# Optimization experiments

Measured on AMD Instinct MI355X. Metric: run time of the kernel, lower is better.

## Reference

```python
import jax, jax.numpy as jnp
import numpy as np

N = 1024
IN_CH = 128
EDGE_CH = 32
OUT_CH = 128


def setup_inputs() -> dict:
    key = jax.random.key(0)
    ks = jax.random.split(key, 8)
    return {
        "node_mat": jax.random.normal(ks[0], (N, IN_CH), dtype=jnp.float32),
        "adj": jax.random.uniform(ks[1], (N, N), dtype=jnp.float32),
        "edge_adj": jax.random.uniform(ks[2], (EDGE_CH, N, N), dtype=jnp.float32),
        "node_weight": jax.random.normal(ks[3], (IN_CH, OUT_CH), dtype=jnp.float32) * 0.05,
        "edge_lay_1": jax.random.normal(ks[4], (EDGE_CH, OUT_CH - 1), dtype=jnp.float32) * 0.05,
        "edge_lay_2": jax.random.normal(ks[5], (OUT_CH - 1, OUT_CH), dtype=jnp.float32) * 0.05,
        "root": jax.random.normal(ks[6], (IN_CH, OUT_CH), dtype=jnp.float32) * 0.05,
        "bias": jax.random.normal(ks[7], (OUT_CH,), dtype=jnp.float32) * 0.05,
    }


def reference(node_mat, adj, edge_adj, node_weight, edge_lay_1, edge_lay_2, root, bias):
    # node message passing: adj-weighted sum of transformed node features  [N, out]
    sum_filter_node_msgs = adj @ (node_mat @ node_weight)
    # edge MLP: 2-layer with ReLU, applied over the edge-channel axis
    # edge_adj: [E, N, N]; edge_lay_1: [E, out-1] -> h1: [out-1, N, N]
    h1 = jnp.maximum(jnp.einsum('enm,eb->bnm', edge_adj, edge_lay_1), 0.0)
    # h1: [out-1, N, N]; edge_lay_2: [out-1, out] -> h2: [out, N, N]
    h2 = jnp.einsum('bnm,bo->onm', h1, edge_lay_2)
    # adjacency-weighted compression: e_compress[n, o] = sum_m h2[o, n, m] * adj[n, m]
    e_compress = jnp.einsum('onm,nm->no', h2, adj)
    root_info = node_mat @ root
    return sum_filter_node_msgs + e_compress + root_info + bias
```

## Files before the change

kernel.cpp:

```cpp
#include <hip/hip_runtime.h>
#include <hip/hip_bf16.h>

#define NN 1024
#define IN_CH 128
#define EDGE_CH 32
#define OUT_CH 128

typedef __attribute__((ext_vector_type(8))) short bf16x8;
typedef __attribute__((ext_vector_type(4))) float f32x4;

static __device__ __forceinline__ short f2bf(float f) {
    union { float f; unsigned u; } v; v.f = f;
    unsigned r = v.u + 0x7FFFu + ((v.u >> 16) & 1u);
    return (short)(r >> 16);
}

__global__ void node_gemm_kernel(const float* __restrict__ node_mat,
                                 const float* __restrict__ node_weight,
                                 const float* __restrict__ root,
                                 short* __restrict__ PT,
                                 float* __restrict__ R) {
    __shared__ float nm[2 * IN_CH];
    int tid = threadIdx.x;
    int n0 = blockIdx.x * 2;
    nm[tid] = node_mat[n0 * IN_CH + tid];
    __syncthreads();
    int o = tid & 127;
    int h = tid >> 7;
    const float* nr = &nm[h * IN_CH];
    float accp = 0.f, accr = 0.f;
#pragma unroll 8
    for (int c = 0; c < IN_CH; ++c) {
        float x = nr[c];
        accp += x * node_weight[c * OUT_CH + o];
        accr += x * root[c * OUT_CH + o];
    }
    R[(size_t)(n0 + h) * OUT_CH + o] = accr;
    PT[(size_t)o * NN + (n0 + h)] = f2bf(accp);
}

__global__ void edge_out_kernel(const float* __restrict__ edge_adj,
                                const float* __restrict__ adj,
                                const float* __restrict__ L1,
                                const float* __restrict__ L2,
                                const float* __restrict__ R,
                                const float* __restrict__ bias,
                                float* __restrict__ out) {
    int n = blockIdx.x;
    int tid = threadIdx.x;
    int wave = tid >> 6;
    int lane = tid & 63;
    int quad = lane >> 4;
    int col  = lane & 15;

    __shared__ short ea_lds[2][128 * 40];
    __shared__ float gred[4][OUT_CH];
    __shared__ float gs[OUT_CH];
    __shared__ float part[2][OUT_CH];

    bf16x8 a_frag[8];
#pragma unroll
    for (int bt = 0; bt < 8; ++bt) {
        int b = bt * 16 + col;
#pragma unroll
        for (int j = 0; j < 8; ++j) {
            int e = quad * 8 + j;
            float v = (b < OUT_CH - 1) ? L1[e * (OUT_CH - 1) + b] : 0.0f;
            a_frag[bt][j] = f2bf(v);
        }
    }

    float g_acc[8][4];
#pragma unroll
    for (int bt = 0; bt < 8; ++bt)
#pragma unroll
        for (int r = 0; r < 4; ++r) g_acc[bt][r] = 0.0f;

    const float* adj_row = adj + (size_t)n * NN;

    int se = tid >> 3;
    int sm = (tid & 7) * 4;
    const float* ea_row = edge_adj + (size_t)se * (size_t)(NN * NN) + (size_t)n * NN;

    f32x4 st[4];
#pragma unroll
    for (int i = 0; i < 4; ++i)
        st[i] = *(const f32x4*)(ea_row + sm + 32 * i);
#pragma unroll
    for (int i = 0; i < 4; ++i)
#pragma unroll
        for (int k = 0; k < 4; ++k)
            ea_lds[0][(sm + 32 * i + k) * 40 + se] = f2bf(st[i][k]);
    __syncthreads();

    for (int c = 0; c < 8; ++c) {
        int cur = c & 1;
        if (c < 7) {
            const float* p = ea_row + (c + 1) * 128;
#pragma unroll
            for (int i = 0; i < 4; ++i)
                st[i] = *(const f32x4*)(p + sm + 32 * i);
        }
        int mloc0 = wave * 32;
#pragma unroll
        for (int s = 0; s < 2; ++s) {
            int mloc = mloc0 + s * 16 + col;
            float adjv = adj_row[c * 128 + mloc];
            bf16x8 bf = *(const bf16x8*)((const char*)&ea_lds[cur][0] +
                                         (size_t)mloc * 80 + quad * 16);
#pragma unroll
            for (int bt = 0; bt < 8; ++bt) {
                f32x4 d = __builtin_amdgcn_mfma_f32_16x16x32_bf16(
                    a_frag[bt], bf, (f32x4){0.f, 0.f, 0.f, 0.f}, 0, 0, 0);
#pragma unroll
                for (int r = 0; r < 4; ++r)
                    g_acc[bt][r] += fmaxf(d[r], 0.0f) * adjv;
            }
        }
        if (c < 7) {
            int nxt = cur ^ 1;
#pragma unroll
            for (int i = 0; i < 4; ++i)
#pragma unroll
                for (int k = 0; k < 4; ++k)
                    ea_lds[nxt][(sm + 32 * i + k) * 40 + se] = f2bf(st[i][k]);
        }
        __syncthreads();
    }

#pragma unroll
    for (int bt = 0; bt < 8; ++bt)
#pragma unroll
        for (int r = 0; r < 4; ++r) {
            float v = g_acc[bt][r];
            v += __shfl_xor(v, 1);
            v += __shfl_xor(v, 2);
            v += __shfl_xor(v, 4);
            v += __shfl_xor(v, 8);
            g_acc[bt][r] = v;
        }

    if (col == 0) {
#pragma unroll
        for (int bt = 0; bt < 8; ++bt)
#pragma unroll
            for (int r = 0; r < 4; ++r)
                gred[wave][bt * 16 + quad * 4 + r] = g_acc[bt][r];
    }
    __syncthreads();
    if (tid < OUT_CH)
        gs[tid] = gred[0][tid] + gred[1][tid] + gred[2][tid] + gred[3][tid];
    __syncthreads();

    int o = tid & 127;
    int hf = tid >> 7;
    float acc = 0.f;
    int blo = hf * 64, bhi = hf ? 127 : 64;
#pragma unroll 8
    for (int b = blo; b < bhi; ++b)
        acc += gs[b] * L2[b * OUT_CH + o];
    part[hf][o] = acc;
    __syncthreads();
    if (tid < 128)
        out[(size_t)n * OUT_CH + tid] =
            part[0][tid] + part[1][tid] + R[(size_t)n * OUT_CH + tid] + bias[tid];
}

__global__ void adjp_kernel(const float* __restrict__ adj,
                            const short* __restrict__ PT,
                            float* __restrict__ out) {
    int blk = blockIdx.x;
    int nb = blk & 63;
    int oh = blk >> 6;
    int tid = threadIdx.x;
    int wave = tid >> 6;
    int lane = tid & 63;
    int quad = lane >> 4;
    int col  = lane & 15;
    int n0 = nb * 16;
    int o0 = oh * 64;

    f32x4 acc[4];
#pragma unroll
    for (int ot = 0; ot < 4; ++ot) acc[ot] = (f32x4){0.f, 0.f, 0.f, 0.f};

    int kbase = wave * 256;
#pragma unroll
    for (int ks = 0; ks < 8; ++ks) {
        int k = kbase + ks * 32 + quad * 8;
        const float* ap = adj + (size_t)(n0 + col) * NN + k;
        f32x4 a0 = *(const f32x4*)ap;
        f32x4 a1 = *(const f32x4*)(ap + 4);
        bf16x8 a;
#pragma unroll
        for (int j = 0; j < 4; ++j) { a[j] = f2bf(a0[j]); a[4 + j] = f2bf(a1[j]); }
#pragma unroll
        for (int ot = 0; ot < 4; ++ot) {
            int o = o0 + ot * 16 + col;
            bf16x8 b = *(const bf16x8*)(PT + (size_t)o * NN + k);
            acc[ot] = __builtin_amdgcn_mfma_f32_16x16x32_bf16(a, b, acc[ot], 0, 0, 0);
        }
    }

    __shared__ float red[4][16][65];
#pragma unroll
    for (int ot = 0; ot < 4; ++ot)
#pragma unroll
        for (int r = 0; r < 4; ++r)
            red[wave][quad * 4 + r][ot * 16 + col] = acc[ot][r];
    __syncthreads();

#pragma unroll
    for (int i = tid; i < 16 * 64; i += 256) {
        int rr = i >> 6;
        int cc = i & 63;
        float v = red[0][rr][cc] + red[1][rr][cc] + red[2][rr][cc] + red[3][rr][cc];
        out[(size_t)(n0 + rr) * OUT_CH + o0 + cc] += v;
    }
}

extern "C" void kernel_launch(void* const* d_in, const int* in_sizes, int n_in,
                              void* d_out, int out_size, void* d_ws, size_t ws_size,
                              hipStream_t stream) {
    const float* node_mat    = (const float*)d_in[0];
    const float* adj         = (const float*)d_in[1];
    const float* edge_adj    = (const float*)d_in[2];
    const float* node_weight = (const float*)d_in[3];
    const float* edge_lay_1  = (const float*)d_in[4];
    const float* edge_lay_2  = (const float*)d_in[5];
    const float* root        = (const float*)d_in[6];
    const float* bias        = (const float*)d_in[7];
    float* out = (float*)d_out;

    short* PT = (short*)d_ws;
    float* R  = (float*)((char*)d_ws + OUT_CH * NN * sizeof(short));

    node_gemm_kernel<<<NN / 2, 256, 0, stream>>>(node_mat, node_weight, root, PT, R);
    edge_out_kernel<<<NN, 256, 0, stream>>>(edge_adj, adj, edge_lay_1, edge_lay_2,
                                            R, bias, out);
    adjp_kernel<<<128, 256, 0, stream>>>(adj, PT, out);
}
```

Measured before the change: 251.2 us.

## Give each wave private LDS staging buffers and deepen edge_adj prefetch

The edge kernel now splits the m-dimension so each wave stages and consumes only its own 256-column slice of edge_adj. It uses per-wave double-buffered LDS regions and wave barriers in place of block-wide __syncthreads. Loads are prefetched two chunks ahead with two register stage sets and the chunk loop is fully unrolled. This is meant to remove block-level synchronization stalls and hide more global latency, at the cost of more registers and smaller per-row load segments (32 floats per edge channel).

Result: slower. 357.3 us (+42.2%).

```diff
diff --git a/kernel.cpp b/kernel.cpp
--- a/kernel.cpp
+++ b/kernel.cpp
@@ -53,7 +53,7 @@
     int quad = lane >> 4;
     int col  = lane & 15;
 
-    __shared__ short ea_lds[2][128 * 40];
+    __shared__ __attribute__((aligned(16))) short ea_lds[4][2][32 * 40];
     __shared__ float gred[4][OUT_CH];
     __shared__ float gs[OUT_CH];
     __shared__ float part[2][OUT_CH];
@@ -77,37 +77,44 @@
         for (int r = 0; r < 4; ++r) g_acc[bt][r] = 0.0f;
 
     const float* adj_row = adj + (size_t)n * NN;
-
-    int se = tid >> 3;
-    int sm = (tid & 7) * 4;
-    const float* ea_row = edge_adj + (size_t)se * (size_t)(NN * NN) + (size_t)n * NN;
-
-    f32x4 st[4];
+    int mw = wave * 256;
+    int eg = lane >> 3;
+    int ml = (lane & 7) * 4;
+    const float* ea_nm = edge_adj + (size_t)n * NN + mw + ml;
+
+    short* buf0 = &ea_lds[wave][0][0];
+    short* buf1 = &ea_lds[wave][1][0];
+
+    f32x4 st[2][4];
 #pragma unroll
     for (int i = 0; i < 4; ++i)
-        st[i] = *(const f32x4*)(ea_row + sm + 32 * i);
+        st[0][i] = *(const f32x4*)(ea_nm + (size_t)(i * 8 + eg) * (size_t)(NN * NN));
 #pragma unroll
     for (int i = 0; i < 4; ++i)
+        st[1][i] = *(const f32x4*)(ea_nm + (size_t)(i * 8 + eg) * (size_t)(NN * NN) + 32);
+#pragma unroll
+    for (int i = 0; i < 4; ++i)
 #pragma unroll
         for (int k = 0; k < 4; ++k)
-            ea_lds[0][(sm + 32 * i + k) * 40 + se] = f2bf(st[i][k]);
-    __syncthreads();
-
+            buf0[(ml + k) * 40 + i * 8 + eg] = f2bf(st[0][i][k]);
+    __builtin_amdgcn_wave_barrier();
+
+#pragma unroll
     for (int c = 0; c < 8; ++c) {
-        int cur = c & 1;
-        if (c < 7) {
-            const float* p = ea_row + (c + 1) * 128;
+        const int cur = c & 1;
+        short* bufc = (cur == 0) ? buf0 : buf1;
+        short* bufn = (cur == 0) ? buf1 : buf0;
+        if (c < 6) {
 #pragma unroll
             for (int i = 0; i < 4; ++i)
-                st[i] = *(const f32x4*)(p + sm + 32 * i);
-        }
-        int mloc0 = wave * 32;
+                st[cur][i] = *(const f32x4*)(ea_nm +
+                    (size_t)(i * 8 + eg) * (size_t)(NN * NN) + (c + 2) * 32);
+        }
 #pragma unroll
         for (int s = 0; s < 2; ++s) {
-            int mloc = mloc0 + s * 16 + col;
-            float adjv = adj_row[c * 128 + mloc];
-            bf16x8 bf = *(const bf16x8*)((const char*)&ea_lds[cur][0] +
-                                         (size_t)mloc * 80 + quad * 16);
+            int mloc = s * 16 + col;
+            float adjv = adj_row[mw + c * 32 + mloc];
+            bf16x8 bf = *(const bf16x8*)(bufc + mloc * 40 + quad * 8);
 #pragma unroll
             for (int bt = 0; bt < 8; ++bt) {
                 f32x4 d = __builtin_amdgcn_mfma_f32_16x16x32_bf16(
@@ -118,14 +125,14 @@
             }
         }
         if (c < 7) {
-            int nxt = cur ^ 1;
+            __builtin_amdgcn_wave_barrier();
 #pragma unroll
             for (int i = 0; i < 4; ++i)
 #pragma unroll
                 for (int k = 0; k < 4; ++k)
-                    ea_lds[nxt][(sm + 32 * i + k) * 40 + se] = f2bf(st[i][k]);
-        }
-        __syncthreads();
+                    bufn[(ml + k) * 40 + i * 8 + eg] = f2bf(st[cur ^ 1][i][k]);
+            __builtin_amdgcn_wave_barrier();
+        }
     }
 
 #pragma unroll
```
